# Performance work log

Hardware: AMD Instinct MI355X
Metric: run time of the kernel (lower is better)

The kernel has to match this reference:

```python
import jax, jax.numpy as jnp
import numpy as np

NC, M, D = 4, 512, 64
COMMITMENT_COST = 0.25


def setup_inputs() -> dict:
    key = jax.random.key(0)
    k1, k2 = jax.random.split(key)
    N = 65536
    x = jax.random.normal(k1, (N, NC * D), dtype=jnp.float32)
    # original init: uniform(-1/m, 1/m); randn*small keeps comparable scale
    embedding = jax.random.normal(k2, (NC, M, D), dtype=jnp.float32) * (1.0 / M)
    mask = jnp.ones((N, NC), dtype=jnp.float32)
    return {"x": x, "embedding": embedding, "mask": mask}


def reference(x, embedding, mask):
    nc, m, d = embedding.shape
    x_flat = x.reshape(-1, nc, d)                      # (N, nc, d)
    xd = jax.lax.stop_gradient(x_flat)                 # detached copy

    # squared-distance search expressed as a GEMM (same math as sum((x-e)^2)):
    x2 = jnp.sum(xd * xd, axis=-1)[:, :, None]
    e2 = jnp.sum(embedding * embedding, axis=-1)[None, :, :]
    xe = jnp.einsum('ncd,cmd->ncm', xd, embedding)
    distances = x2 - 2.0 * xe + e2

    indices = jnp.argmin(distances, axis=-1)           # (N, nc) int
    # gather nearest code vectors: (N, nc, d)
    quantized = embedding[jnp.arange(nc)[None, :], indices]
    quantized = quantized * mask[..., None]

    codebook_loss = jnp.mean((jax.lax.stop_gradient(x_flat) - quantized) ** 2)
    e_latent_loss = jnp.mean((x_flat - jax.lax.stop_gradient(quantized)) ** 2)
    commitment_loss = COMMITMENT_COST * e_latent_loss

    # straight-through estimator
    quantized_st = x_flat + jax.lax.stop_gradient(quantized - x_flat)
    quantized_st = quantized_st.reshape(x.shape)

    # perplexity via per-codebook histogram (avoids N x nc x m one-hot)
    counts = jax.vmap(lambda idx: jnp.bincount(idx, length=m))(indices.T)  # (nc, m)
    avg_probs = counts.astype(x.dtype) / x_flat.shape[0]
    perplexity = jnp.exp(-jnp.sum(avg_probs * jnp.log(avg_probs + 1e-10)))

    return (quantized_st, commitment_loss, codebook_loss, perplexity, indices)
```

## Files before the change

kernel.cpp:

```cpp
#include <hip/hip_runtime.h>
#include <math.h>
#include <float.h>

#define NTOK 65536
#define NCB  4
#define MCODE 512
#define DIM  64

#define QST_SIZE (NTOK * NCB * DIM)
#define IDX_OFF  (QST_SIZE + 3)

#define TOK_TILE  256

#define WS_EH 0
#define WS_EL 262144
#define WS_D0 524288
#define WS_CNT 532480
#define WS_LOSS 540672

typedef _Float16 half8 __attribute__((ext_vector_type(8)));
typedef float floatx4 __attribute__((ext_vector_type(4)));

__global__ __launch_bounds__(256) void prep_kernel(const float* __restrict__ emb,
                                                   _Float16* __restrict__ eh,
                                                   _Float16* __restrict__ el,
                                                   float* __restrict__ d0,
                                                   int* __restrict__ counts,
                                                   float* __restrict__ lossSum) {
    int row = blockIdx.x * 256 + threadIdx.x;
    if (row >= NCB * MCODE) return;
    const float* src = emb + (size_t)row * DIM;
    _Float16* ph = eh + (size_t)row * DIM;
    _Float16* pl = el + (size_t)row * DIM;
    float s = 0.f;
#pragma unroll
    for (int j = 0; j < DIM / 8; ++j) {
        half8 h, l;
#pragma unroll
        for (int t = 0; t < 8; ++t) {
            float e = src[j * 8 + t];
            s += e * e;
            float f = e * 512.0f;
            _Float16 hi = (_Float16)f;
            float r = f - (float)hi;
            h[t] = hi;
            l[t] = (_Float16)r;
        }
        *(half8*)(ph + j * 8) = h;
        *(half8*)(pl + j * 8) = l;
    }
    d0[row] = 512.0f * s;
    counts[row] = 0;
    if (row == 0) *lossSum = 0.f;
}

__global__ __launch_bounds__(256) void vq_main(const float* __restrict__ x,
                                               const float* __restrict__ emb,
                                               const float* __restrict__ mask,
                                               const _Float16* __restrict__ eh,
                                               const _Float16* __restrict__ el,
                                               const float* __restrict__ d0,
                                               int* __restrict__ counts,
                                               float* __restrict__ lossSum,
                                               float* __restrict__ outQ,
                                               float* __restrict__ outIdx) {
    __shared__ int   Is[TOK_TILE];
    __shared__ float wls[4];

    const int tid  = threadIdx.x;
    const int c    = blockIdx.y;
    const int n0tk = blockIdx.x * TOK_TILE;
    const int lane = tid & 63;
    const int w    = tid >> 6;
    const int col  = lane & 15;
    const int quad = lane >> 4;

    half8 Ahi[4][2], Alo[4][2];
#pragma unroll
    for (int s = 0; s < 4; ++s) {
        const float* xr = x + (size_t)(n0tk + w * 64 + s * 16 + col) * (NCB * DIM) + c * DIM;
#pragma unroll
        for (int ks = 0; ks < 2; ++ks) {
            const float* p = xr + ks * 32 + quad * 8;
            float4 f0 = *(const float4*)(p);
            float4 f1 = *(const float4*)(p + 4);
            float fv[8] = {f0.x, f0.y, f0.z, f0.w, f1.x, f1.y, f1.z, f1.w};
            half8 h, l;
#pragma unroll
            for (int t = 0; t < 8; ++t) {
                _Float16 hi = (_Float16)fv[t];
                float r = fv[t] - (float)hi;
                h[t] = hi;
                l[t] = (_Float16)r;
            }
            Ahi[s][ks] = h;
            Alo[s][ks] = l;
        }
    }

    float minv[4][4];
    int   mini[4][4];
#pragma unroll
    for (int s = 0; s < 4; ++s)
#pragma unroll
        for (int r = 0; r < 4; ++r) { minv[s][r] = FLT_MAX; mini[s][r] = 0; }

    const _Float16* ehc = eh + (size_t)c * MCODE * DIM + (size_t)col * DIM + quad * 8;
    const _Float16* elc = el + (size_t)c * MCODE * DIM + (size_t)col * DIM + quad * 8;
    const float*    d0c = d0 + c * MCODE;

    half8 Bh0 = *(const half8*)(ehc);
    half8 Bh1 = *(const half8*)(ehc + 32);
    half8 Bl0 = *(const half8*)(elc);
    half8 Bl1 = *(const half8*)(elc + 32);
    float d0v = d0c[col];

    for (int nt = 0; nt < 32; ++nt) {
        const int n = nt * 16 + col;
        half8 Ch0, Ch1, Cl0, Cl1; float d0n;
        if (nt < 31) {
            const _Float16* bh = ehc + (size_t)(nt + 1) * 16 * DIM;
            const _Float16* bl = elc + (size_t)(nt + 1) * 16 * DIM;
            Ch0 = *(const half8*)(bh);
            Ch1 = *(const half8*)(bh + 32);
            Cl0 = *(const half8*)(bl);
            Cl1 = *(const half8*)(bl + 32);
            d0n = d0c[(nt + 1) * 16 + col];
        }
#pragma unroll
        for (int s = 0; s < 4; ++s) {
            floatx4 acc = {0.f, 0.f, 0.f, 0.f};
            acc = __builtin_amdgcn_mfma_f32_16x16x32_f16(Ahi[s][0], Bh0, acc, 0, 0, 0);
            acc = __builtin_amdgcn_mfma_f32_16x16x32_f16(Ahi[s][1], Bh1, acc, 0, 0, 0);
            acc = __builtin_amdgcn_mfma_f32_16x16x32_f16(Alo[s][0], Bh0, acc, 0, 0, 0);
            acc = __builtin_amdgcn_mfma_f32_16x16x32_f16(Alo[s][1], Bh1, acc, 0, 0, 0);
            acc = __builtin_amdgcn_mfma_f32_16x16x32_f16(Ahi[s][0], Bl0, acc, 0, 0, 0);
            acc = __builtin_amdgcn_mfma_f32_16x16x32_f16(Ahi[s][1], Bl1, acc, 0, 0, 0);
#pragma unroll
            for (int r = 0; r < 4; ++r) {
                float dv = fmaf(-2.f, acc[r], d0v);
                if (dv < minv[s][r]) { minv[s][r] = dv; mini[s][r] = n; }
            }
        }
        if (nt < 31) {
            Bh0 = Ch0; Bh1 = Ch1; Bl0 = Cl0; Bl1 = Cl1; d0v = d0n;
        }
    }

#pragma unroll
    for (int off = 1; off < 16; off <<= 1) {
#pragma unroll
        for (int s = 0; s < 4; ++s)
#pragma unroll
            for (int r = 0; r < 4; ++r) {
                float ov = __shfl_xor(minv[s][r], off);
                int   oi = __shfl_xor(mini[s][r], off);
                if (ov < minv[s][r] || (ov == minv[s][r] && oi < mini[s][r])) {
                    minv[s][r] = ov; mini[s][r] = oi;
                }
            }
    }
    if (col == 0) {
#pragma unroll
        for (int s = 0; s < 4; ++s)
#pragma unroll
            for (int r = 0; r < 4; ++r)
                Is[w * 64 + s * 16 + quad * 4 + r] = mini[s][r];
    }
    __syncthreads();

    {
        int idx = Is[tid];
        atomicAdd(&counts[c * MCODE + idx], 1);
        outIdx[(size_t)(n0tk + tid) * NCB + c] = (float)idx;
    }

    float lloss = 0.f;
#pragma unroll
    for (int i = 0; i < 16; ++i) {
        int q = tid + i * 256;
        int tok = q >> 4, d4 = q & 15;
        int idx = Is[tok];
        float mv = mask[(size_t)(n0tk + tok) * NCB + c];
        float4 e4 = *(const float4*)(emb + ((size_t)c * MCODE + idx) * DIM + d4 * 4);
        float4 x4 = *(const float4*)(x + (size_t)(n0tk + tok) * (NCB * DIM) + c * DIM + d4 * 4);
        float qx = e4.x * mv, qy = e4.y * mv, qz = e4.z * mv, qw = e4.w * mv;
        float4 o;
        o.x = x4.x + (qx - x4.x);
        o.y = x4.y + (qy - x4.y);
        o.z = x4.z + (qz - x4.z);
        o.w = x4.w + (qw - x4.w);
        *(float4*)(outQ + (size_t)(n0tk + tok) * (NCB * DIM) + c * DIM + d4 * 4) = o;
        float dx = x4.x - qx, dy = x4.y - qy, dz = x4.z - qz, dw = x4.w - qw;
        lloss += dx * dx + dy * dy + dz * dz + dw * dw;
    }
#pragma unroll
    for (int off = 32; off > 0; off >>= 1) lloss += __shfl_xor(lloss, off);
    if ((tid & 63) == 0) wls[tid >> 6] = lloss;
    __syncthreads();
    if (tid == 0) {
        float s = wls[0] + wls[1] + wls[2] + wls[3];
        atomicAdd(lossSum, s);
    }
}

__global__ __launch_bounds__(256) void finalize_kernel(const int* __restrict__ counts,
                                                       const float* __restrict__ lossSum,
                                                       float* __restrict__ out) {
    __shared__ float wls[4];
    int tid = threadIdx.x;
    float s = 0.f;
#pragma unroll
    for (int i = 0; i < 8; ++i) {
        int j = tid + i * 256;
        float p = (float)counts[j] * (1.0f / 65536.0f);
        s += p * logf(p + 1e-10f);
    }
#pragma unroll
    for (int off = 32; off > 0; off >>= 1) s += __shfl_xor(s, off);
    if ((tid & 63) == 0) wls[tid >> 6] = s;
    __syncthreads();
    if (tid == 0) {
        float tot = wls[0] + wls[1] + wls[2] + wls[3];
        float L = *lossSum * (1.0f / (float)QST_SIZE);
        out[QST_SIZE + 0] = 0.25f * L;
        out[QST_SIZE + 1] = L;
        out[QST_SIZE + 2] = expf(-tot);
    }
}

extern "C" void kernel_launch(void* const* d_in, const int* in_sizes, int n_in,
                              void* d_out, int out_size, void* d_ws, size_t ws_size,
                              hipStream_t stream) {
    const float* x    = (const float*)d_in[0];
    const float* emb  = (const float*)d_in[1];
    const float* mask = (const float*)d_in[2];
    float* out = (float*)d_out;

    _Float16* eh   = (_Float16*)((char*)d_ws + WS_EH);
    _Float16* el   = (_Float16*)((char*)d_ws + WS_EL);
    float* d0      = (float*)((char*)d_ws + WS_D0);
    int*   counts  = (int*)((char*)d_ws + WS_CNT);
    float* lossSum = (float*)((char*)d_ws + WS_LOSS);

    prep_kernel<<<dim3(8), dim3(256), 0, stream>>>(emb, eh, el, d0, counts, lossSum);
    vq_main<<<dim3(NTOK / TOK_TILE, NCB), dim3(256), 0, stream>>>(
        x, emb, mask, eh, el, d0, counts, lossSum, out, out + IDX_OFF);
    finalize_kernel<<<dim3(1), dim3(256), 0, stream>>>(counts, lossSum, out);
}
```

Before: 228.6 us.

## Halve token tile, fuse finalize via last-block counter, parallelize prep

Halves the token tile per block to 128, doubling the grid to 2048 blocks, and adds a launch-bounds occupancy hint so more waves fit per CU. The separate finalize kernel is folded into vq_main: a done counter picks the last block to finish, which computes perplexity and the losses, saving one launch. The prep kernel now spreads each embedding row across 16 threads with a shuffle reduction instead of one thread per row. In exchange, each embedding tile loaded from cache is reused by fewer tokens, and the last-block pattern adds a fence and atomics.

```diff
diff --git a/kernel.cpp b/kernel.cpp
--- a/kernel.cpp
+++ b/kernel.cpp
@@ -10,15 +10,18 @@
 #define QST_SIZE (NTOK * NCB * DIM)
 #define IDX_OFF  (QST_SIZE + 3)
 
-#define TOK_TILE  256
+#define TOK_TILE  128
+#define NBLOCKS   (NTOK / TOK_TILE * NCB)
 
 #define WS_EH 0
 #define WS_EL 262144
 #define WS_D0 524288
 #define WS_CNT 532480
 #define WS_LOSS 540672
+#define WS_DONE 540676
 
 typedef _Float16 half8 __attribute__((ext_vector_type(8)));
+typedef _Float16 half4 __attribute__((ext_vector_type(4)));
 typedef float floatx4 __attribute__((ext_vector_type(4)));
 
 __global__ __launch_bounds__(256) void prep_kernel(const float* __restrict__ emb,
@@ -26,46 +29,47 @@
                                                    _Float16* __restrict__ el,
                                                    float* __restrict__ d0,
                                                    int* __restrict__ counts,
-                                                   float* __restrict__ lossSum) {
-    int row = blockIdx.x * 256 + threadIdx.x;
-    if (row >= NCB * MCODE) return;
-    const float* src = emb + (size_t)row * DIM;
-    _Float16* ph = eh + (size_t)row * DIM;
-    _Float16* pl = el + (size_t)row * DIM;
-    float s = 0.f;
-#pragma unroll
-    for (int j = 0; j < DIM / 8; ++j) {
-        half8 h, l;
-#pragma unroll
-        for (int t = 0; t < 8; ++t) {
-            float e = src[j * 8 + t];
-            s += e * e;
-            float f = e * 512.0f;
-            _Float16 hi = (_Float16)f;
-            float r = f - (float)hi;
-            h[t] = hi;
-            l[t] = (_Float16)r;
-        }
-        *(half8*)(ph + j * 8) = h;
-        *(half8*)(pl + j * 8) = l;
-    }
-    d0[row] = 512.0f * s;
-    counts[row] = 0;
-    if (row == 0) *lossSum = 0.f;
+                                                   float* __restrict__ lossSum,
+                                                   unsigned* __restrict__ done) {
+    const int tid = threadIdx.x;
+    const int d4  = tid & 15;
+#pragma unroll
+    for (int p = 0; p < 4; ++p) {
+        int row = blockIdx.x * 64 + p * 16 + (tid >> 4);
+        float4 v = *(const float4*)(emb + (size_t)row * DIM + d4 * 4);
+        float s = v.x * v.x + v.y * v.y + v.z * v.z + v.w * v.w;
+        half4 h, l;
+        float f0 = v.x * 512.0f, f1 = v.y * 512.0f, f2 = v.z * 512.0f, f3 = v.w * 512.0f;
+        h[0] = (_Float16)f0; l[0] = (_Float16)(f0 - (float)h[0]);
+        h[1] = (_Float16)f1; l[1] = (_Float16)(f1 - (float)h[1]);
+        h[2] = (_Float16)f2; l[2] = (_Float16)(f2 - (float)h[2]);
+        h[3] = (_Float16)f3; l[3] = (_Float16)(f3 - (float)h[3]);
+        *(half4*)(eh + (size_t)row * DIM + d4 * 4) = h;
+        *(half4*)(el + (size_t)row * DIM + d4 * 4) = l;
+#pragma unroll
+        for (int off = 1; off < 16; off <<= 1) s += __shfl_xor(s, off);
+        if (d4 == 0) {
+            d0[row] = 512.0f * s;
+            counts[row] = 0;
+        }
+    }
+    if (blockIdx.x == 0 && tid == 0) { *lossSum = 0.f; *done = 0u; }
 }
 
-__global__ __launch_bounds__(256) void vq_main(const float* __restrict__ x,
-                                               const float* __restrict__ emb,
-                                               const float* __restrict__ mask,
-                                               const _Float16* __restrict__ eh,
-                                               const _Float16* __restrict__ el,
-                                               const float* __restrict__ d0,
-                                               int* __restrict__ counts,
-                                               float* __restrict__ lossSum,
-                                               float* __restrict__ outQ,
-                                               float* __restrict__ outIdx) {
+__global__ __launch_bounds__(256, 6) void vq_main(const float* __restrict__ x,
+                                                  const float* __restrict__ emb,
+                                                  const float* __restrict__ mask,
+                                                  const _Float16* __restrict__ eh,
+                                                  const _Float16* __restrict__ el,
+                                                  const float* __restrict__ d0,
+                                                  int* __restrict__ counts,
+                                                  float* __restrict__ lossSum,
+                                                  unsigned* __restrict__ done,
+                                                  float* __restrict__ outQ,
+                                                  float* __restrict__ outIdx) {
     __shared__ int   Is[TOK_TILE];
     __shared__ float wls[4];
+    __shared__ int   lastFlag;
 
     const int tid  = threadIdx.x;
     const int c    = blockIdx.y;
@@ -75,10 +79,10 @@
     const int col  = lane & 15;
     const int quad = lane >> 4;
 
-    half8 Ahi[4][2], Alo[4][2];
-#pragma unroll
-    for (int s = 0; s < 4; ++s) {
-        const float* xr = x + (size_t)(n0tk + w * 64 + s * 16 + col) * (NCB * DIM) + c * DIM;
+    half8 Ahi[2][2], Alo[2][2];
+#pragma unroll
+    for (int s = 0; s < 2; ++s) {
+        const float* xr = x + (size_t)(n0tk + w * 32 + s * 16 + col) * (NCB * DIM) + c * DIM;
 #pragma unroll
         for (int ks = 0; ks < 2; ++ks) {
             const float* p = xr + ks * 32 + quad * 8;
@@ -98,10 +102,10 @@
         }
     }
 
-    float minv[4][4];
-    int   mini[4][4];
-#pragma unroll
-    for (int s = 0; s < 4; ++s)
+    float minv[2][4];
+    int   mini[2][4];
+#pragma unroll
+    for (int s = 0; s < 2; ++s)
 #pragma unroll
         for (int r = 0; r < 4; ++r) { minv[s][r] = FLT_MAX; mini[s][r] = 0; }
 
@@ -128,7 +132,7 @@
             d0n = d0c[(nt + 1) * 16 + col];
         }
 #pragma unroll
-        for (int s = 0; s < 4; ++s) {
+        for (int s = 0; s < 2; ++s) {
             floatx4 acc = {0.f, 0.f, 0.f, 0.f};
             acc = __builtin_amdgcn_mfma_f32_16x16x32_f16(Ahi[s][0], Bh0, acc, 0, 0, 0);
             acc = __builtin_amdgcn_mfma_f32_16x16x32_f16(Ahi[s][1], Bh1, acc, 0, 0, 0);
@@ -150,7 +154,7 @@
 #pragma unroll
     for (int off = 1; off < 16; off <<= 1) {
 #pragma unroll
-        for (int s = 0; s < 4; ++s)
+        for (int s = 0; s < 2; ++s)
 #pragma unroll
             for (int r = 0; r < 4; ++r) {
                 float ov = __shfl_xor(minv[s][r], off);
@@ -162,14 +166,14 @@
     }
     if (col == 0) {
 #pragma unroll
-        for (int s = 0; s < 4; ++s)
+        for (int s = 0; s < 2; ++s)
 #pragma unroll
             for (int r = 0; r < 4; ++r)
-                Is[w * 64 + s * 16 + quad * 4 + r] = mini[s][r];
+                Is[w * 32 + s * 16 + quad * 4 + r] = mini[s][r];
     }
     __syncthreads();
 
-    {
+    if (tid < TOK_TILE) {
         int idx = Is[tid];
         atomicAdd(&counts[c * MCODE + idx], 1);
         outIdx[(size_t)(n0tk + tid) * NCB + c] = (float)idx;
@@ -177,7 +181,7 @@
 
     float lloss = 0.f;
 #pragma unroll
-    for (int i = 0; i < 16; ++i) {
+    for (int i = 0; i < 8; ++i) {
         int q = tid + i * 256;
         int tok = q >> 4, d4 = q & 15;
         int idx = Is[tok];
@@ -201,31 +205,32 @@
     if (tid == 0) {
         float s = wls[0] + wls[1] + wls[2] + wls[3];
         atomicAdd(lossSum, s);
-    }
-}
-
-__global__ __launch_bounds__(256) void finalize_kernel(const int* __restrict__ counts,
-                                                       const float* __restrict__ lossSum,
-                                                       float* __restrict__ out) {
-    __shared__ float wls[4];
-    int tid = threadIdx.x;
-    float s = 0.f;
-#pragma unroll
-    for (int i = 0; i < 8; ++i) {
-        int j = tid + i * 256;
-        float p = (float)counts[j] * (1.0f / 65536.0f);
-        s += p * logf(p + 1e-10f);
-    }
-#pragma unroll
-    for (int off = 32; off > 0; off >>= 1) s += __shfl_xor(s, off);
-    if ((tid & 63) == 0) wls[tid >> 6] = s;
+        __threadfence();
+        unsigned o = atomicAdd(done, 1u);
+        lastFlag = (o == (unsigned)(NBLOCKS - 1)) ? 1 : 0;
+    }
     __syncthreads();
-    if (tid == 0) {
-        float tot = wls[0] + wls[1] + wls[2] + wls[3];
-        float L = *lossSum * (1.0f / (float)QST_SIZE);
-        out[QST_SIZE + 0] = 0.25f * L;
-        out[QST_SIZE + 1] = L;
-        out[QST_SIZE + 2] = expf(-tot);
+
+    if (lastFlag) {
+        float s = 0.f;
+#pragma unroll
+        for (int i = 0; i < 8; ++i) {
+            int j = tid + i * 256;
+            int cnt = atomicAdd(&counts[j], 0);
+            float p = (float)cnt * (1.0f / 65536.0f);
+            s += p * logf(p + 1e-10f);
+        }
+#pragma unroll
+        for (int off = 32; off > 0; off >>= 1) s += __shfl_xor(s, off);
+        if ((tid & 63) == 0) wls[tid >> 6] = s;
+        __syncthreads();
+        if (tid == 0) {
+            float tot = wls[0] + wls[1] + wls[2] + wls[3];
+            float L = atomicAdd(lossSum, 0.f) * (1.0f / (float)QST_SIZE);
+            outQ[QST_SIZE + 0] = 0.25f * L;
+            outQ[QST_SIZE + 1] = L;
+            outQ[QST_SIZE + 2] = expf(-tot);
+        }
     }
 }
 
@@ -237,14 +242,14 @@
     const float* mask = (const float*)d_in[2];
     float* out = (float*)d_out;
 
-    _Float16* eh   = (_Float16*)((char*)d_ws + WS_EH);
-    _Float16* el   = (_Float16*)((char*)d_ws + WS_EL);
-    float* d0      = (float*)((char*)d_ws + WS_D0);
-    int*   counts  = (int*)((char*)d_ws + WS_CNT);
-    float* lossSum = (float*)((char*)d_ws + WS_LOSS);
-
-    prep_kernel<<<dim3(8), dim3(256), 0, stream>>>(emb, eh, el, d0, counts, lossSum);
+    _Float16* eh     = (_Float16*)((char*)d_ws + WS_EH);
+    _Float16* el     = (_Float16*)((char*)d_ws + WS_EL);
+    float* d0        = (float*)((char*)d_ws + WS_D0);
+    int*   counts    = (int*)((char*)d_ws + WS_CNT);
+    float* lossSum   = (float*)((char*)d_ws + WS_LOSS);
+    unsigned* doneCt = (unsigned*)((char*)d_ws + WS_DONE);
+
+    prep_kernel<<<dim3(32), dim3(256), 0, stream>>>(emb, eh, el, d0, counts, lossSum, doneCt);
     vq_main<<<dim3(NTOK / TOK_TILE, NCB), dim3(256), 0, stream>>>(
-        x, emb, mask, eh, el, d0, counts, lossSum, out, out + IDX_OFF);
-    finalize_kernel<<<dim3(1), dim3(256), 0, stream>>>(counts, lossSum, out);
+        x, emb, mask, eh, el, d0, counts, lossSum, doneCt, out, out + IDX_OFF);
 }
```

After: 336.6 us. +47.2%, slower.
